# Kernel tuning notes

Measured on AMD Instinct MI355X. Metric: run time of the kernel, lower is better.

## Reference

```python
import jax, jax.numpy as jnp
import numpy as np
from jax import lax

B = 16
C_IN = 103      # image_channels / conv_inputs (spectral bands)
H = W = 9       # patch size
C_CONV = 256    # conv_outputs == primary_unit_size (in_size of routing)
N_PRIM = 32     # num_primary_units (in_units, contracted dim)
N_OUT = 103     # num_output_units
D_OUT = 16      # output_unit_size
N_ITER = 3
REC = H * W * C_IN          # 8343
H1 = int(REC * 2 / 3)       # 5562
H2 = int(REC * 3 / 2)       # 12514


def squash(s, axis):
    # torch: mag_sq/(1+mag_sq) * s/mag, reduced over `axis`
    mag_sq = jnp.sum(s * s, axis=axis, keepdims=True)
    mag = jnp.sqrt(mag_sq)
    return mag_sq / (1.0 + mag_sq) * (s / mag)


def setup_inputs() -> dict:
    key = jax.random.key(0)
    ks = jax.random.split(key, 10)
    x = jax.random.normal(ks[0], (B, C_IN, H, W), jnp.float32)
    conv_w = 0.05 * jax.random.normal(ks[1], (C_CONV, C_IN, 3, 3), jnp.float32)
    conv_b = jnp.zeros((C_CONV,), jnp.float32)
    # torch: nn.Parameter(torch.randn(1, in_size, out_units, out_size, in_units)); drop leading 1
    W_caps = jax.random.normal(ks[2], (C_CONV, N_OUT, D_OUT, N_PRIM), jnp.float32)
    fc1_w = 0.02 * jax.random.normal(ks[3], (N_OUT * D_OUT, H1), jnp.float32)
    fc1_b = jnp.zeros((H1,), jnp.float32)
    fc2_w = 0.02 * jax.random.normal(ks[4], (H1, H2), jnp.float32)
    fc2_b = jnp.zeros((H2,), jnp.float32)
    fc3_w = 0.02 * jax.random.normal(ks[5], (H2, REC), jnp.float32)
    fc3_b = jnp.zeros((REC,), jnp.float32)
    return {"x": x, "conv_w": conv_w, "conv_b": conv_b, "W_caps": W_caps,
            "fc1_w": fc1_w, "fc1_b": fc1_b, "fc2_w": fc2_w, "fc2_b": fc2_b,
            "fc3_w": fc3_w, "fc3_b": fc3_b}


def reference(x, conv_w, conv_b, W_caps, fc1_w, fc1_b, fc2_w, fc2_b, fc3_w, fc3_b):
    # ConvLayer: 3x3 valid conv + relu -> [B, C_CONV, 7, 7]
    h = lax.conv_general_dilated(x, conv_w, (1, 1), 'VALID',
                                 dimension_numbers=('NCHW', 'OIHW', 'NCHW'))
    h = jax.nn.relu(h + conv_b[None, :, None, None])

    # PrimaryCapsuleLayer: N_PRIM identical AdaptiveAvgPool2d(1) units
    p = h.mean(axis=(2, 3))                                   # [B, C_CONV]
    u = jnp.broadcast_to(p[:, None, :], (B, N_PRIM, C_CONV))  # [B, N_PRIM, C_CONV]
    u = squash(u, axis=2)

    # CapsuleLayer dynamic routing
    xt = u.transpose(0, 2, 1)                                 # [B, C_CONV, N_PRIM]
    # u_hat[b,c,j,o] = sum_i W[c,j,o,i] * xt[b,c,i]
    u_hat = jnp.einsum('cjoi,bci->bcjo', W_caps, xt)          # [B, C_CONV, N_OUT, D_OUT]

    b_ij = jnp.ones((1, C_CONV, N_OUT, 1), u_hat.dtype)
    v_j = None
    for _ in range(N_ITER):
        c_ij = jax.nn.softmax(b_ij, axis=1)                   # softmax over in_size
        s_j = jnp.sum(c_ij * u_hat, axis=1, keepdims=True)    # [B, 1, N_OUT, D_OUT]
        v_j = squash(s_j, axis=2)                             # torch squashes over out_units dim
        agree = jnp.sum(u_hat * v_j, axis=3, keepdims=True)   # [B, C_CONV, N_OUT, 1]
        b_ij = b_ij + agree.mean(axis=0, keepdims=True)

    v = v_j[:, 0]                                             # [B, N_OUT, D_OUT]
    # band_attention = ||v_j||_2 over out_size, shape [B, N_OUT, 1, 1] (torch)
    ba = jnp.linalg.norm(v, axis=-1, keepdims=True)[..., None]

    # ReconstructionLayer on attention-weighted capsules
    f = (v * ba[..., 0]).reshape(B, -1)                       # [B, N_OUT*D_OUT]
    f = f @ fc1_w + fc1_b
    f = f @ fc2_w + fc2_b
    f = f @ fc3_w + fc3_b
    recon = f.reshape(B, C_IN, H, W)
    return ba, recon
```

## Files before the change

kernel.cpp:

```cpp
#include <hip/hip_runtime.h>
#include <math.h>

#define BATCH 16
#define CIN 103
#define CCONV 256
#define NOUT 103
#define DOUT 16
#define RECSZ 8343
#define H1SZ 5562
#define H2SZ 12514

#define WS_P      0
#define WS_SQ     4096
#define WS_WSUM   8192
#define WS_BB     430080
#define WS_S      456448
#define WS_FACTOR 482816
#define WS_F0     483072
#define WS_F1     509440
#define WS_F2     598432
#define WS_PART1  798656
#define WS_PART2  4536320
#define WS_PART3  12345056

__global__ __launch_bounds__(256) void init_bb_k(float* __restrict__ bb) {
    int i = blockIdx.x * 256 + threadIdx.x;
    if (i < 103 * 256) bb[i] = 1.0f;
}

__global__ __launch_bounds__(256) void conv_pool_k(const float* __restrict__ x,
                                                   const float* __restrict__ w,
                                                   const float* __restrict__ cb,
                                                   float* __restrict__ p) {
    int b = blockIdx.x >> 6;
    int cob = (blockIdx.x & 63) << 2;
    __shared__ float xs[CIN * 81];
    int t = threadIdx.x;
    for (int i = t; i < CIN * 81; i += 256) xs[i] = x[(size_t)b * CIN * 81 + i];
    __syncthreads();
    int wave = t >> 6, lane = t & 63;
    int co = cob + wave;
    co = __builtin_amdgcn_readfirstlane(co);
    int pos = lane < 49 ? lane : 0;
    int oh = pos / 7, ow = pos % 7;
    const float* wp = w + (size_t)co * CIN * 9;
    const float* xp = xs + oh * 9 + ow;
    float acc = 0.f;
    for (int ci = 0; ci < CIN; ++ci) {
#pragma unroll
        for (int kh = 0; kh < 3; ++kh)
#pragma unroll
            for (int kw = 0; kw < 3; ++kw)
                acc = fmaf(xp[ci * 81 + kh * 9 + kw], wp[ci * 9 + kh * 3 + kw], acc);
    }
    acc += cb[co];
    acc = fmaxf(acc, 0.f);
    if (lane >= 49) acc = 0.f;
#pragma unroll
    for (int off = 32; off; off >>= 1) acc += __shfl_down(acc, off);
    if (lane == 0) p[b * 256 + co] = acc * (1.0f / 49.0f);
}

__global__ __launch_bounds__(256) void squash_p_k(const float* __restrict__ p, float* __restrict__ sq) {
    int b = blockIdx.x, c = threadIdx.x;
    float v = p[b * 256 + c];
    float ss = v * v;
#pragma unroll
    for (int off = 32; off; off >>= 1) ss += __shfl_down(ss, off);
    __shared__ float red[4];
    if ((c & 63) == 0) red[c >> 6] = ss;
    __syncthreads();
    float ms = red[0] + red[1] + red[2] + red[3];
    float mag = sqrtf(ms);
    sq[b * 256 + c] = v * mag / (1.f + ms);
}

__global__ __launch_bounds__(256) void wsum_k(const float* __restrict__ Wc, float* __restrict__ wsum) {
    int idx = blockIdx.x * 256 + threadIdx.x;
    const float4* p4 = (const float4*)(Wc + (size_t)idx * 32);
    float s = 0.f;
#pragma unroll
    for (int q = 0; q < 8; ++q) { float4 v = p4[q]; s += v.x + v.y + v.z + v.w; }
    wsum[idx] = s;
}

__global__ __launch_bounds__(256) void route_s_k(const float* __restrict__ sq,
                                                 const float* __restrict__ wsum,
                                                 const float* __restrict__ bb,
                                                 float* __restrict__ s_out) {
    int j = blockIdx.x;
    int t = threadIdx.x;
    __shared__ float sqst[4096];
    __shared__ float wls[4096];
    __shared__ float cc[256];
    __shared__ float red[8];
    float bv = bb[j * 256 + t];
    for (int i = t; i < 4096; i += 256) {
        sqst[i] = sq[((i & 15) << 8) + (i >> 4)];
        wls[i] = wsum[(size_t)(i >> 4) * (103 * 16) + j * 16 + (i & 15)];
    }
    int wave = t >> 6, lane = t & 63;
    float m = bv;
#pragma unroll
    for (int off = 32; off; off >>= 1) m = fmaxf(m, __shfl_down(m, off));
    if (lane == 0) red[wave] = m;
    __syncthreads();
    m = fmaxf(fmaxf(red[0], red[1]), fmaxf(red[2], red[3]));
    float e = expf(bv - m);
    float ssum = e;
#pragma unroll
    for (int off = 32; off; off >>= 1) ssum += __shfl_down(ssum, off);
    if (lane == 0) red[4 + wave] = ssum;
    __syncthreads();
    ssum = red[4] + red[5] + red[6] + red[7];
    cc[t] = e / ssum;
    __syncthreads();
    for (int i = t; i < 4096; i += 256) sqst[i] *= cc[i >> 4];
    __syncthreads();
    int b = t >> 4, o = t & 15;
    float acc = 0.f;
    for (int c = 0; c < 256; ++c)
        acc = fmaf(sqst[c * 16 + b], wls[c * 16 + o], acc);
    s_out[((size_t)b * 103 + j) * 16 + o] = acc;
}

__global__ __launch_bounds__(256) void factor_k(const float* __restrict__ s, float* __restrict__ factor) {
    int t = threadIdx.x;
    int b = t >> 4, o = t & 15;
    float ms = 0.f;
    for (int j = 0; j < 103; ++j) {
        float v = s[((size_t)b * 103 + j) * 16 + o];
        ms = fmaf(v, v, ms);
    }
    factor[t] = sqrtf(ms) / (1.f + ms);
}

__global__ __launch_bounds__(256) void route_upd_k(const float* __restrict__ sq,
                                                   const float* __restrict__ wsum,
                                                   const float* __restrict__ s,
                                                   const float* __restrict__ factor,
                                                   float* __restrict__ bb) {
    int j = blockIdx.x;
    int t = threadIdx.x;
    __shared__ float vs[256];
    {
        int b = t >> 4, o = t & 15;
        vs[t] = s[((size_t)b * 103 + j) * 16 + o] * factor[t];
    }
    __syncthreads();
    const float4* wp = (const float4*)(wsum + ((size_t)t * 103 + j) * 16);
    float4 w0 = wp[0], w1 = wp[1], w2 = wp[2], w3 = wp[3];
    float wv[16] = {w0.x, w0.y, w0.z, w0.w, w1.x, w1.y, w1.z, w1.w,
                    w2.x, w2.y, w2.z, w2.w, w3.x, w3.y, w3.z, w3.w};
    float acc = 0.f;
#pragma unroll
    for (int b = 0; b < 16; ++b) {
        float d = 0.f;
#pragma unroll
        for (int o = 0; o < 16; ++o) d = fmaf(wv[o], vs[b * 16 + o], d);
        acc = fmaf(sq[b * 256 + t], d, acc);
    }
    bb[j * 256 + t] += acc * (1.0f / 16.0f);
}

__global__ __launch_bounds__(256) void final_v_k(const float* __restrict__ s,
                                                 const float* __restrict__ factor,
                                                 float* __restrict__ out_ba,
                                                 float* __restrict__ f0t) {
    int idx = blockIdx.x * 256 + threadIdx.x;
    if (idx >= 16 * 103) return;
    int b = idx / 103;
    int j = idx - b * 103;
    const float4* sp = (const float4*)(s + (size_t)idx * 16);
    float4 s0 = sp[0], s1 = sp[1], s2 = sp[2], s3 = sp[3];
    float sv[16] = {s0.x, s0.y, s0.z, s0.w, s1.x, s1.y, s1.z, s1.w,
                    s2.x, s2.y, s2.z, s2.w, s3.x, s3.y, s3.z, s3.w};
    float v[16];
    float nrm2 = 0.f;
#pragma unroll
    for (int o = 0; o < 16; ++o) {
        v[o] = sv[o] * factor[b * 16 + o];
        nrm2 = fmaf(v[o], v[o], nrm2);
    }
    float ba = sqrtf(nrm2);
    out_ba[idx] = ba;
    float* fp = f0t + ((size_t)j << 8) + b;
#pragma unroll
    for (int o = 0; o < 16; ++o) fp[o << 4] = v[o] * ba;
}

template <bool V2, bool OUT_T>
__global__ __launch_bounds__(256) void fc_k(const float* __restrict__ in,
                                            const float* __restrict__ w,
                                            float* __restrict__ part,
                                            int K, int N, int kchunk) {
    extern __shared__ float sact[];
    const int k0 = blockIdx.y * kchunk;
    int nk = K - k0; if (nk > kchunk) nk = kchunk;
    for (int i = threadIdx.x; i < (nk << 4); i += 256)
        sact[i] = in[((size_t)k0 << 4) + i];
    __syncthreads();

    const int c0 = blockIdx.x * 512 + (threadIdx.x << 1);
    const bool st0 = c0 < N;
    const bool st1 = c0 + 1 < N;
    const int c = st0 ? c0 : 0;
    const int off1 = st1 ? 1 : 0;
    const float* wp = w + (size_t)k0 * N + c;
    const size_t Ns = (size_t)N;

    float a0[16], a1[16];
#pragma unroll
    for (int b = 0; b < 16; ++b) { a0[b] = 0.f; a1[b] = 0.f; }

    int k = 0;
    for (; k + 4 <= nk; k += 4) {
        float w00, w01, w10, w11, w20, w21, w30, w31;
        if (V2) {
            float2 q0 = *(const float2*)(wp);
            float2 q1 = *(const float2*)(wp + Ns);
            float2 q2 = *(const float2*)(wp + 2 * Ns);
            float2 q3 = *(const float2*)(wp + 3 * Ns);
            w00 = q0.x; w01 = q0.y; w10 = q1.x; w11 = q1.y;
            w20 = q2.x; w21 = q2.y; w30 = q3.x; w31 = q3.y;
        } else {
            w00 = wp[0];          w01 = wp[off1];
            w10 = wp[Ns];         w11 = wp[Ns + off1];
            w20 = wp[2 * Ns];     w21 = wp[2 * Ns + off1];
            w30 = wp[3 * Ns];     w31 = wp[3 * Ns + off1];
        }
        wp += 4 * Ns;
        const float* s0 = sact + (k << 4);
#pragma unroll
        for (int b = 0; b < 16; ++b) {
            float v0 = s0[b], v1 = s0[16 + b], v2 = s0[32 + b], v3 = s0[48 + b];
            a0[b] = fmaf(v0, w00, a0[b]);
            a1[b] = fmaf(v0, w01, a1[b]);
            a0[b] = fmaf(v1, w10, a0[b]);
            a1[b] = fmaf(v1, w11, a1[b]);
            a0[b] = fmaf(v2, w20, a0[b]);
            a1[b] = fmaf(v2, w21, a1[b]);
            a0[b] = fmaf(v3, w30, a0[b]);
            a1[b] = fmaf(v3, w31, a1[b]);
        }
    }
    for (; k < nk; ++k) {
        float wv0, wv1;
        if (V2) { float2 q = *(const float2*)(wp); wv0 = q.x; wv1 = q.y; }
        else    { wv0 = wp[0]; wv1 = wp[off1]; }
        wp += Ns;
        const float* s0 = sact + (k << 4);
#pragma unroll
        for (int b = 0; b < 16; ++b) {
            a0[b] = fmaf(s0[b], wv0, a0[b]);
            a1[b] = fmaf(s0[b], wv1, a1[b]);
        }
    }

    float* po = part + (size_t)blockIdx.y * (Ns << 4);
    if (OUT_T) {
        if (st0) {
            float* q = po + ((size_t)c << 4);
#pragma unroll
            for (int b = 0; b < 16; ++b) q[b] = a0[b];
        }
        if (st1) {
            float* q = po + ((size_t)(c + 1) << 4);
#pragma unroll
            for (int b = 0; b < 16; ++b) q[b] = a1[b];
        }
    } else {
        if (st0) {
#pragma unroll
            for (int b = 0; b < 16; ++b) po[(size_t)b * Ns + c] = a0[b];
        }
        if (st1) {
#pragma unroll
            for (int b = 0; b < 16; ++b) po[(size_t)b * Ns + c + 1] = a1[b];
        }
    }
}

template <bool T>
__global__ __launch_bounds__(256) void fcred_k(const float* __restrict__ P,
                                               const float* __restrict__ bias,
                                               float* __restrict__ out,
                                               int total, int ny, int N) {
    int i = blockIdx.x * 256 + threadIdx.x;
    if (i >= total) return;
    float sv = T ? bias[i >> 4] : bias[i % N];
    const float* p = P + i;
    for (int y = 0; y < ny; ++y) sv += p[(size_t)y * total];
    out[i] = sv;
}

extern "C" void kernel_launch(void* const* d_in, const int* in_sizes, int n_in,
                              void* d_out, int out_size, void* d_ws, size_t ws_size,
                              hipStream_t stream) {
    const float* x      = (const float*)d_in[0];
    const float* conv_w = (const float*)d_in[1];
    const float* conv_b = (const float*)d_in[2];
    const float* W_caps = (const float*)d_in[3];
    const float* fc1_w  = (const float*)d_in[4];
    const float* fc1_b  = (const float*)d_in[5];
    const float* fc2_w  = (const float*)d_in[6];
    const float* fc2_b  = (const float*)d_in[7];
    const float* fc3_w  = (const float*)d_in[8];
    const float* fc3_b  = (const float*)d_in[9];
    float* out = (float*)d_out;
    float* ws  = (float*)d_ws;

    float* p      = ws + WS_P;
    float* sq     = ws + WS_SQ;
    float* wsum   = ws + WS_WSUM;
    float* bb     = ws + WS_BB;
    float* s      = ws + WS_S;
    float* factor = ws + WS_FACTOR;
    float* f0     = ws + WS_F0;
    float* f1     = ws + WS_F1;
    float* f2     = ws + WS_F2;
    float* part1  = ws + WS_PART1;
    float* part2  = ws + WS_PART2;
    float* part3  = ws + WS_PART3;
    float* ba_out = out;
    float* recon  = out + 1648;

    init_bb_k<<<103, 256, 0, stream>>>(bb);

    conv_pool_k<<<1024, 256, 0, stream>>>(x, conv_w, conv_b, p);
    squash_p_k<<<16, 256, 0, stream>>>(p, sq);
    wsum_k<<<1648, 256, 0, stream>>>(W_caps, wsum);

    for (int it = 0; it < 3; ++it) {
        route_s_k<<<103, 256, 0, stream>>>(sq, wsum, bb, s);
        factor_k<<<1, 256, 0, stream>>>(s, factor);
        if (it < 2)
            route_upd_k<<<103, 256, 0, stream>>>(sq, wsum, s, factor, bb);
    }
    final_v_k<<<7, 256, 0, stream>>>(s, factor, ba_out, f0);

    fc_k<true, true><<<dim3(11, 42), 256, 40 * 64, stream>>>(f0, fc1_w, part1, 1648, H1SZ, 40);
    fcred_k<true><<<348, 256, 0, stream>>>(part1, fc1_b, f1, 16 * H1SZ, 42, H1SZ);

    fc_k<true, true><<<dim3(25, 39), 256, 144 * 64, stream>>>(f1, fc2_w, part2, H1SZ, H2SZ, 144);
    fcred_k<true><<<783, 256, 0, stream>>>(part2, fc2_b, f2, 16 * H2SZ, 39, H2SZ);

    fc_k<false, false><<<dim3(17, 61), 256, 208 * 64, stream>>>(f2, fc3_w, part3, H2SZ, RECSZ, 208);
    fcred_k<false><<<522, 256, 0, stream>>>(part3, fc3_b, recon, 16 * RECSZ, 61, RECSZ);
}
```

Baseline: 986.2 us.

## Fuse squash factor into routing kernels and read FC activations directly from global

Removes the single-block factor_k launch by recomputing the squash factor inside route_upd_k and final_v_k. Each block redundantly reduces over all 103 output units to get it. The FC kernels no longer stage the activation chunk in shared memory and instead read it straight from global memory as uniform broadcast loads through the cache. This drops launches and a barrier plus LDS traffic in the weight-streaming FC kernels. The cost is redundant global reads, and activation loads that may add latency in the inner FMA loop.

```diff
diff --git a/kernel.cpp b/kernel.cpp
--- a/kernel.cpp
+++ b/kernel.cpp
@@ -15,7 +15,6 @@
 #define WS_WSUM   8192
 #define WS_BB     430080
 #define WS_S      456448
-#define WS_FACTOR 482816
 #define WS_F0     483072
 #define WS_F1     509440
 #define WS_F2     598432
@@ -124,28 +123,22 @@
     s_out[((size_t)b * 103 + j) * 16 + o] = acc;
 }
 
-__global__ __launch_bounds__(256) void factor_k(const float* __restrict__ s, float* __restrict__ factor) {
-    int t = threadIdx.x;
-    int b = t >> 4, o = t & 15;
-    float ms = 0.f;
-    for (int j = 0; j < 103; ++j) {
-        float v = s[((size_t)b * 103 + j) * 16 + o];
-        ms = fmaf(v, v, ms);
-    }
-    factor[t] = sqrtf(ms) / (1.f + ms);
-}
-
 __global__ __launch_bounds__(256) void route_upd_k(const float* __restrict__ sq,
                                                    const float* __restrict__ wsum,
                                                    const float* __restrict__ s,
-                                                   const float* __restrict__ factor,
                                                    float* __restrict__ bb) {
     int j = blockIdx.x;
     int t = threadIdx.x;
     __shared__ float vs[256];
     {
         int b = t >> 4, o = t & 15;
-        vs[t] = s[((size_t)b * 103 + j) * 16 + o] * factor[t];
+        float ms = 0.f;
+        for (int j2 = 0; j2 < 103; ++j2) {
+            float v = s[((size_t)b * 103 + j2) * 16 + o];
+            ms = fmaf(v, v, ms);
+        }
+        float fac = sqrtf(ms) / (1.f + ms);
+        vs[t] = s[((size_t)b * 103 + j) * 16 + o] * fac;
     }
     __syncthreads();
     const float4* wp = (const float4*)(wsum + ((size_t)t * 103 + j) * 16);
@@ -164,10 +157,21 @@
 }
 
 __global__ __launch_bounds__(256) void final_v_k(const float* __restrict__ s,
-                                                 const float* __restrict__ factor,
                                                  float* __restrict__ out_ba,
                                                  float* __restrict__ f0t) {
-    int idx = blockIdx.x * 256 + threadIdx.x;
+    __shared__ float fac[256];
+    int t = threadIdx.x;
+    {
+        int b = t >> 4, o = t & 15;
+        float ms = 0.f;
+        for (int j = 0; j < 103; ++j) {
+            float v = s[((size_t)b * 103 + j) * 16 + o];
+            ms = fmaf(v, v, ms);
+        }
+        fac[t] = sqrtf(ms) / (1.f + ms);
+    }
+    __syncthreads();
+    int idx = blockIdx.x * 256 + t;
     if (idx >= 16 * 103) return;
     int b = idx / 103;
     int j = idx - b * 103;
@@ -179,7 +183,7 @@
     float nrm2 = 0.f;
 #pragma unroll
     for (int o = 0; o < 16; ++o) {
-        v[o] = sv[o] * factor[b * 16 + o];
+        v[o] = sv[o] * fac[b * 16 + o];
         nrm2 = fmaf(v[o], v[o], nrm2);
     }
     float ba = sqrtf(nrm2);
@@ -194,12 +198,8 @@
                                             const float* __restrict__ w,
                                             float* __restrict__ part,
                                             int K, int N, int kchunk) {
-    extern __shared__ float sact[];
     const int k0 = blockIdx.y * kchunk;
     int nk = K - k0; if (nk > kchunk) nk = kchunk;
-    for (int i = threadIdx.x; i < (nk << 4); i += 256)
-        sact[i] = in[((size_t)k0 << 4) + i];
-    __syncthreads();
 
     const int c0 = blockIdx.x * 512 + (threadIdx.x << 1);
     const bool st0 = c0 < N;
@@ -207,6 +207,7 @@
     const int c = st0 ? c0 : 0;
     const int off1 = st1 ? 1 : 0;
     const float* wp = w + (size_t)k0 * N + c;
+    const float* ap = in + ((size_t)k0 << 4);
     const size_t Ns = (size_t)N;
 
     float a0[16], a1[16];
@@ -230,10 +231,10 @@
             w30 = wp[3 * Ns];     w31 = wp[3 * Ns + off1];
         }
         wp += 4 * Ns;
-        const float* s0 = sact + (k << 4);
+        const float* a = ap + (k << 4);
 #pragma unroll
         for (int b = 0; b < 16; ++b) {
-            float v0 = s0[b], v1 = s0[16 + b], v2 = s0[32 + b], v3 = s0[48 + b];
+            float v0 = a[b], v1 = a[16 + b], v2 = a[32 + b], v3 = a[48 + b];
             a0[b] = fmaf(v0, w00, a0[b]);
             a1[b] = fmaf(v0, w01, a1[b]);
             a0[b] = fmaf(v1, w10, a0[b]);
@@ -249,11 +250,11 @@
         if (V2) { float2 q = *(const float2*)(wp); wv0 = q.x; wv1 = q.y; }
         else    { wv0 = wp[0]; wv1 = wp[off1]; }
         wp += Ns;
-        const float* s0 = sact + (k << 4);
+        const float* a = ap + (k << 4);
 #pragma unroll
         for (int b = 0; b < 16; ++b) {
-            a0[b] = fmaf(s0[b], wv0, a0[b]);
-            a1[b] = fmaf(s0[b], wv1, a1[b]);
+            a0[b] = fmaf(a[b], wv0, a0[b]);
+            a1[b] = fmaf(a[b], wv1, a1[b]);
         }
     }
 
@@ -315,7 +316,6 @@
     float* wsum   = ws + WS_WSUM;
     float* bb     = ws + WS_BB;
     float* s      = ws + WS_S;
-    float* factor = ws + WS_FACTOR;
     float* f0     = ws + WS_F0;
     float* f1     = ws + WS_F1;
     float* f2     = ws + WS_F2;
@@ -333,18 +333,17 @@
 
     for (int it = 0; it < 3; ++it) {
         route_s_k<<<103, 256, 0, stream>>>(sq, wsum, bb, s);
-        factor_k<<<1, 256, 0, stream>>>(s, factor);
         if (it < 2)
-            route_upd_k<<<103, 256, 0, stream>>>(sq, wsum, s, factor, bb);
-    }
-    final_v_k<<<7, 256, 0, stream>>>(s, factor, ba_out, f0);
-
-    fc_k<true, true><<<dim3(11, 42), 256, 40 * 64, stream>>>(f0, fc1_w, part1, 1648, H1SZ, 40);
+            route_upd_k<<<103, 256, 0, stream>>>(sq, wsum, s, bb);
+    }
+    final_v_k<<<7, 256, 0, stream>>>(s, ba_out, f0);
+
+    fc_k<true, true><<<dim3(11, 42), 256, 0, stream>>>(f0, fc1_w, part1, 1648, H1SZ, 40);
     fcred_k<true><<<348, 256, 0, stream>>>(part1, fc1_b, f1, 16 * H1SZ, 42, H1SZ);
 
-    fc_k<true, true><<<dim3(25, 39), 256, 144 * 64, stream>>>(f1, fc2_w, part2, H1SZ, H2SZ, 144);
+    fc_k<true, true><<<dim3(25, 39), 256, 0, stream>>>(f1, fc2_w, part2, H1SZ, H2SZ, 144);
     fcred_k<true><<<783, 256, 0, stream>>>(part2, fc2_b, f2, 16 * H2SZ, 39, H2SZ);
 
-    fc_k<false, false><<<dim3(17, 61), 256, 208 * 64, stream>>>(f2, fc3_w, part3, H2SZ, RECSZ, 208);
+    fc_k<false, false><<<dim3(17, 61), 256, 0, stream>>>(f2, fc3_w, part3, H2SZ, RECSZ, 208);
     fcred_k<false><<<522, 256, 0, stream>>>(part3, fc3_b, recon, 16 * RECSZ, 61, RECSZ);
 }
```

Measured after the change: 944.0 us. 1.04x faster.
